# Kernel optimization log

Measured on AMD Instinct MI355X. Metric: run time of the kernel, lower is better.

## Reference

```python
import jax, jax.numpy as jnp
import numpy as np
from jax import lax


def quick_gelu(x):
    return x * jax.nn.sigmoid(1.702 * x)


def setup_inputs() -> dict:
    key = jax.random.key(0)
    ks = jax.random.split(key, 12)
    B, H, W, C, D, M = 32, 56, 56, 192, 64, 8
    g = lambda k, shape, s: (jax.random.normal(k, shape, jnp.float32) * s)
    return {
        "x": jax.random.normal(ks[0], (B, H, W, C), jnp.float32),
        "W1": g(ks[1], (64, C), 0.05),
        "b1": jnp.zeros((64,), jnp.float32),
        "W2": g(ks[2], (64, 64), 0.05),
        "b2": jnp.zeros((64,), jnp.float32),
        "mask_token": g(ks[3], (M, 64), 0.05),
        "Wh": g(ks[4], (D * D * 9, 64), 0.02),
        "bh": g(ks[5], (D * D * 9,), 0.02),
        "Wd": g(ks[6], (D, C), 0.05),
        "bd": jnp.zeros((D,), jnp.float32),
        "Wu": g(ks[7], (C, D), 0.02),
        "bu": jnp.zeros((C,), jnp.float32),
    }


def reference(x, W1, b1, W2, b2, mask_token, Wh, bh, Wd, bd, Wu, bu):
    B, H, W_, C = x.shape
    D = Wd.shape[0]
    M = mask_token.shape[0]
    # meta_net: Linear -> ReLU -> Linear, [B,H,W,64]
    pf = jax.nn.relu(jnp.einsum("bhwc,kc->bhwk", x, W1) + b1)
    pf = jnp.einsum("bhwk,jk->bhwj", pf, W2) + b2
    # mask routing: [M,B,H,W], softmax over spatial positions
    mask = jnp.einsum("bhwk,mk->mbhw", pf, mask_token)
    mask = jax.nn.softmax(mask.reshape(M, B, -1), axis=-1).reshape(M, B, H, W_)
    # sum_m mask[m][...,None]*pf, then sum over H,W -> [B,64]
    mwf = (mask.sum(0)[..., None] * pf).sum(axis=(1, 2))
    # hypernet: per-sample conv weights [B,D,D,3,3]
    conv_w = (jnp.einsum("bk,ok->bo", mwf, Wh) + bh).reshape(B, D, D, 3, 3)
    # adapter_down + QuickGELU, [B,D,H,W]
    xd = jnp.einsum("bhwc,dc->bhwd", x, Wd) + bd
    xp = quick_gelu(xd.transpose(0, 3, 1, 2))

    def conv1(xi, wi):  # xi [D,H,W], wi [D,D,3,3]
        return lax.conv_general_dilated(xi[None], wi, (1, 1), [(1, 1), (1, 1)])[0]

    xc = jax.vmap(conv1)(xp, conv_w)  # [B,D,H,W]
    xd2 = quick_gelu(xc.transpose(0, 2, 3, 1))  # [B,H,W,D]
    # dropout(p=0.1) is identity in eval mode
    xu = jnp.einsum("bhwd,cd->bhwc", xd2, Wu) + bu
    return xu + x
```

## Files before the change

kernel.cpp:

```cpp
#include <hip/hip_runtime.h>

typedef unsigned short ushort_t;
typedef short bf16x8 __attribute__((ext_vector_type(8)));
typedef float f32x4 __attribute__((ext_vector_type(4)));

#define MFMA(a, b, c) __builtin_amdgcn_mfma_f32_16x16x32_bf16(a, b, c, 0, 0, 0)

#define B_    32
#define HW_   3136
#define NPOS  100352

__device__ __forceinline__ float bf2f(unsigned short h) {
    return __uint_as_float(((unsigned int)h) << 16);
}
__device__ __forceinline__ unsigned short f2bf(float f) {
    unsigned int u = __float_as_uint(f);
    u += 0x7FFFu + ((u >> 16) & 1u);
    return (unsigned short)(u >> 16);
}
__device__ __forceinline__ float qgelu(float v) {
    return v / (1.0f + __expf(-1.702f * v));
}
__device__ __forceinline__ void unpack8(uint4 v, float* f) {
    f[0] = bf2f((unsigned short)(v.x & 0xffff)); f[1] = bf2f((unsigned short)(v.x >> 16));
    f[2] = bf2f((unsigned short)(v.y & 0xffff)); f[3] = bf2f((unsigned short)(v.y >> 16));
    f[4] = bf2f((unsigned short)(v.z & 0xffff)); f[5] = bf2f((unsigned short)(v.z >> 16));
    f[6] = bf2f((unsigned short)(v.w & 0xffff)); f[7] = bf2f((unsigned short)(v.w >> 16));
}

__global__ __launch_bounds__(256) void k0_prep(
    const float* __restrict__ W1, const float* __restrict__ W2,
    const float* __restrict__ mtok, const float* __restrict__ Wd,
    const float* __restrict__ Wu,
    ushort_t* __restrict__ w1f, ushort_t* __restrict__ wdf,
    ushort_t* __restrict__ w2f, ushort_t* __restrict__ mtf,
    ushort_t* __restrict__ wuf)
{
    const int gid = blockIdx.x * 256 + threadIdx.x;
    const int stride = gridDim.x * 256;
    for (int i = gid; i < 12288; i += stride) {
        int j = i & 7, lane = (i >> 3) & 63, nt = (i >> 9) & 3, kc = i >> 11;
        int n = nt * 16 + (lane & 15), k = kc * 32 + (lane >> 4) * 8 + j;
        w1f[i] = f2bf(W1[n * 192 + k]);
        wdf[i] = f2bf(Wd[n * 192 + k]);
    }
    for (int i = gid; i < 4096; i += stride) {
        int j = i & 7, lane = (i >> 3) & 63, nt = (i >> 9) & 3, kc = i >> 11;
        int n = nt * 16 + (lane & 15), k = kc * 32 + (lane >> 4) * 8 + j;
        w2f[i] = f2bf(W2[n * 64 + k]);
    }
    for (int i = gid; i < 1024; i += stride) {
        int j = i & 7, lane = (i >> 3) & 63, kc = i >> 9;
        int n = lane & 15, k = kc * 32 + (lane >> 4) * 8 + j;
        mtf[i] = (n < 8) ? f2bf(mtok[n * 64 + k]) : (ushort_t)0;
    }
    for (int i = gid; i < 12288; i += stride) {
        int j = i & 7, lane = (i >> 3) & 63, g = i >> 9;
        int nt = g % 12, kc = g / 12;
        int n = nt * 16 + (lane & 15), k = kc * 32 + (lane >> 4) * 8 + j;
        wuf[i] = f2bf(Wu[n * 64 + k]);
    }
}

__global__ __launch_bounds__(256) void k1_meta_adapter(
    const float* __restrict__ x, const float* __restrict__ b1,
    const float* __restrict__ b2, const float* __restrict__ bd,
    const ushort_t* __restrict__ w1f, const ushort_t* __restrict__ wdf,
    const ushort_t* __restrict__ w2f, const ushort_t* __restrict__ mtf,
    ushort_t* __restrict__ pf2g, ushort_t* __restrict__ xpg,
    float* __restrict__ Lg)
{
    __shared__ ushort_t xs[64 * 200];
    __shared__ ushort_t pf1s[4][16 * 72];

    const int tid = threadIdx.x;
    const int posBase = blockIdx.x * 64;

    #pragma unroll
    for (int t = 0; t < 6; t++) {
        int u = tid + t * 256;
        int pos = u / 24, c8 = u % 24;
        const float4* gp = (const float4*)(x + ((size_t)(posBase + pos)) * 192 + c8 * 8);
        float4 v0 = gp[0], v1 = gp[1];
        bf16x8 r;
        r[0] = (short)f2bf(v0.x); r[1] = (short)f2bf(v0.y);
        r[2] = (short)f2bf(v0.z); r[3] = (short)f2bf(v0.w);
        r[4] = (short)f2bf(v1.x); r[5] = (short)f2bf(v1.y);
        r[6] = (short)f2bf(v1.z); r[7] = (short)f2bf(v1.w);
        *(bf16x8*)&xs[pos * 200 + c8 * 8] = r;
    }
    __syncthreads();

    const int lane = tid & 63, wv = tid >> 6;
    const int col = lane & 15, q = lane >> 4;

    bf16x8 A[6];
    #pragma unroll
    for (int kc = 0; kc < 6; kc++)
        A[kc] = *(const bf16x8*)&xs[(wv * 16 + col) * 200 + kc * 32 + q * 8];

    f32x4 acc1[4], acc3[4];
    #pragma unroll
    for (int nt = 0; nt < 4; nt++) { acc1[nt] = (f32x4)0.0f; acc3[nt] = (f32x4)0.0f; }

    #pragma unroll
    for (int kc = 0; kc < 6; kc++) {
        #pragma unroll
        for (int nt = 0; nt < 4; nt++) {
            bf16x8 B1 = *(const bf16x8*)(w1f + ((kc * 4 + nt) * 64 + lane) * 8);
            acc1[nt] = MFMA(A[kc], B1, acc1[nt]);
            bf16x8 Bd = *(const bf16x8*)(wdf + ((kc * 4 + nt) * 64 + lane) * 8);
            acc3[nt] = MFMA(A[kc], Bd, acc3[nt]);
        }
    }
    __syncthreads();

    #pragma unroll
    for (int nt = 0; nt < 4; nt++) {
        float bias = b1[nt * 16 + col];
        #pragma unroll
        for (int r = 0; r < 4; r++) {
            float v = acc1[nt][r] + bias;
            v = v > 0.0f ? v : 0.0f;
            pf1s[wv][(q * 4 + r) * 72 + nt * 16 + col] = f2bf(v);
        }
    }

    f32x4 acc2[4];
    #pragma unroll
    for (int nt = 0; nt < 4; nt++) acc2[nt] = (f32x4)0.0f;
    #pragma unroll
    for (int kc = 0; kc < 2; kc++) {
        bf16x8 A2 = *(const bf16x8*)&pf1s[wv][col * 72 + kc * 32 + q * 8];
        #pragma unroll
        for (int nt = 0; nt < 4; nt++) {
            bf16x8 B2 = *(const bf16x8*)(w2f + ((kc * 4 + nt) * 64 + lane) * 8);
            acc2[nt] = MFMA(A2, B2, acc2[nt]);
        }
    }

    #pragma unroll
    for (int nt = 0; nt < 4; nt++) {
        float bias = bd[nt * 16 + col];
        #pragma unroll
        for (int r = 0; r < 4; r++) {
            float v = qgelu(acc3[nt][r] + bias);
            xs[(wv * 16 + q * 4 + r) * 72 + nt * 16 + col] = f2bf(v);
        }
    }

    #pragma unroll
    for (int nt = 0; nt < 4; nt++) {
        float bias = b2[nt * 16 + col];
        #pragma unroll
        for (int r = 0; r < 4; r++)
            pf1s[wv][(q * 4 + r) * 72 + nt * 16 + col] = f2bf(acc2[nt][r] + bias);
    }

    f32x4 Lacc = (f32x4)0.0f;
    #pragma unroll
    for (int kc = 0; kc < 2; kc++) {
        bf16x8 A3 = *(const bf16x8*)&pf1s[wv][col * 72 + kc * 32 + q * 8];
        bf16x8 Bm = *(const bf16x8*)(mtf + (kc * 64 + lane) * 8);
        Lacc = MFMA(A3, Bm, Lacc);
    }
    if (col < 8) {
        #pragma unroll
        for (int r = 0; r < 4; r++)
            Lg[((size_t)(posBase + wv * 16 + q * 4 + r)) * 8 + col] = Lacc[r];
    }
    __syncthreads();

    #pragma unroll
    for (int t = 0; t < 2; t++) {
        int u = tid + t * 256;
        int pos = u >> 3, c8 = u & 7;
        uint4 vx = *(const uint4*)&xs[pos * 72 + c8 * 8];
        *(uint4*)(xpg + ((size_t)(posBase + pos)) * 64 + c8 * 8) = vx;
        uint4 vp = *(const uint4*)&pf1s[pos >> 4][(pos & 15) * 72 + c8 * 8];
        *(uint4*)(pf2g + ((size_t)(posBase + pos)) * 64 + c8 * 8) = vp;
    }
}

__global__ __launch_bounds__(256) void k2_mask_mwf(
    const float* __restrict__ Lg, const ushort_t* __restrict__ pf2g,
    float* __restrict__ mwfg)
{
    __shared__ float masksum[HW_];
    __shared__ float wred[4][8];
    __shared__ float smx[8];
    __shared__ float sinv[8];
    __shared__ float sred[32 * 64];

    const int tid = threadIdx.x;
    const int b = blockIdx.x;
    const int lane = tid & 63, wv = tid >> 6;
    const float* Lb = Lg + (size_t)b * HW_ * 8;

    float lmax[8];
    #pragma unroll
    for (int m = 0; m < 8; m++) lmax[m] = -1e30f;
    for (int p = tid; p < HW_; p += 256) {
        const float4* lp = (const float4*)(Lb + (size_t)p * 8);
        float4 a = lp[0], c = lp[1];
        lmax[0] = fmaxf(lmax[0], a.x); lmax[1] = fmaxf(lmax[1], a.y);
        lmax[2] = fmaxf(lmax[2], a.z); lmax[3] = fmaxf(lmax[3], a.w);
        lmax[4] = fmaxf(lmax[4], c.x); lmax[5] = fmaxf(lmax[5], c.y);
        lmax[6] = fmaxf(lmax[6], c.z); lmax[7] = fmaxf(lmax[7], c.w);
    }
    #pragma unroll
    for (int m = 0; m < 8; m++) {
        float v = lmax[m];
        for (int off = 32; off > 0; off >>= 1) v = fmaxf(v, __shfl_down(v, off));
        lmax[m] = v;
    }
    if (lane == 0) {
        #pragma unroll
        for (int m = 0; m < 8; m++) wred[wv][m] = lmax[m];
    }
    __syncthreads();
    if (tid < 8)
        smx[tid] = fmaxf(fmaxf(wred[0][tid], wred[1][tid]), fmaxf(wred[2][tid], wred[3][tid]));
    __syncthreads();

    float lsum[8];
    #pragma unroll
    for (int m = 0; m < 8; m++) lsum[m] = 0.0f;
    for (int p = tid; p < HW_; p += 256) {
        const float4* lp = (const float4*)(Lb + (size_t)p * 8);
        float4 a = lp[0], c = lp[1];
        lsum[0] += __expf(a.x - smx[0]); lsum[1] += __expf(a.y - smx[1]);
        lsum[2] += __expf(a.z - smx[2]); lsum[3] += __expf(a.w - smx[3]);
        lsum[4] += __expf(c.x - smx[4]); lsum[5] += __expf(c.y - smx[5]);
        lsum[6] += __expf(c.z - smx[6]); lsum[7] += __expf(c.w - smx[7]);
    }
    #pragma unroll
    for (int m = 0; m < 8; m++) {
        float v = lsum[m];
        for (int off = 32; off > 0; off >>= 1) v += __shfl_down(v, off);
        lsum[m] = v;
    }
    __syncthreads();
    if (lane == 0) {
        #pragma unroll
        for (int m = 0; m < 8; m++) wred[wv][m] = lsum[m];
    }
    __syncthreads();
    if (tid < 8)
        sinv[tid] = 1.0f / (wred[0][tid] + wred[1][tid] + wred[2][tid] + wred[3][tid]);
    __syncthreads();

    for (int p = tid; p < HW_; p += 256) {
        const float4* lp = (const float4*)(Lb + (size_t)p * 8);
        float4 a = lp[0], c = lp[1];
        float ms = __expf(a.x - smx[0]) * sinv[0] + __expf(a.y - smx[1]) * sinv[1]
                 + __expf(a.z - smx[2]) * sinv[2] + __expf(a.w - smx[3]) * sinv[3]
                 + __expf(c.x - smx[4]) * sinv[4] + __expf(c.y - smx[5]) * sinv[5]
                 + __expf(c.z - smx[6]) * sinv[6] + __expf(c.w - smx[7]) * sinv[7];
        masksum[p] = ms;
    }
    __syncthreads();

    const int part = tid >> 3, kg = tid & 7;
    float a8[8];
    #pragma unroll
    for (int j = 0; j < 8; j++) a8[j] = 0.0f;
    for (int p = part; p < HW_; p += 32) {
        float ms = masksum[p];
        uint4 v = *(const uint4*)(pf2g + ((size_t)b * HW_ + p) * 64 + kg * 8);
        float f[8]; unpack8(v, f);
        #pragma unroll
        for (int j = 0; j < 8; j++) a8[j] += ms * f[j];
    }
    #pragma unroll
    for (int j = 0; j < 8; j++) sred[part * 64 + kg * 8 + j] = a8[j];
    __syncthreads();
    if (tid < 64) {
        float s = 0.0f;
        #pragma unroll
        for (int pt = 0; pt < 32; pt++) s += sred[pt * 64 + tid];
        mwfg[b * 64 + tid] = s;
    }
}

__global__ __launch_bounds__(256) void k3_hypernet(
    const float* __restrict__ mwfg, const float* __restrict__ Whg,
    const float* __restrict__ bhg, ushort_t* __restrict__ cwb)
{
    __shared__ float mwfs[32 * 64];
    const int tid = threadIdx.x;
    for (int i = tid; i < 2048; i += 256) mwfs[i] = mwfg[i];
    __syncthreads();

    const int op = blockIdx.x * 256 + tid;
    const int j = op & 7, lane = (op >> 3) & 63, nt = (op >> 9) & 3;
    const int kc = (op >> 11) & 1, tap = op >> 12;
    const int oc = nt * 16 + (lane & 15);
    const int ic = kc * 32 + (lane >> 4) * 8 + j;
    const int o = oc * 576 + ic * 9 + tap;

    float wreg[64];
    const float4* src = (const float4*)(Whg + (size_t)o * 64);
    #pragma unroll
    for (int t = 0; t < 16; t++) {
        float4 v = src[t];
        wreg[t * 4 + 0] = v.x; wreg[t * 4 + 1] = v.y;
        wreg[t * 4 + 2] = v.z; wreg[t * 4 + 3] = v.w;
    }
    const float bias = bhg[o];
    for (int b = 0; b < 32; b++) {
        float a = bias;
        #pragma unroll
        for (int k = 0; k < 64; k++) a += mwfs[b * 64 + k] * wreg[k];
        cwb[(size_t)b * 36864 + op] = f2bf(a);
    }
}

__global__ __launch_bounds__(256, 4) void k4_conv(
    const ushort_t* __restrict__ xpg, const ushort_t* __restrict__ cwb,
    ushort_t* __restrict__ xd2g)
{
    __shared__ ushort_t xs[2 * 232 * 40];

    const int tid = threadIdx.x;
    const int bid = blockIdx.x;
    const int swz = (bid & 7) * 112 + (bid >> 3);
    const int b = swz / 28, yt = swz % 28, y0 = yt * 2;

    for (int u = tid; u < 1856; u += 256) {
        int r = u / 464, rem = u % 464, c = rem >> 3, c8 = rem & 7;
        int gy = y0 - 1 + r, gx = c - 1;
        uint4 v = make_uint4(0, 0, 0, 0);
        if (gy >= 0 && gy < 56 && gx >= 0 && gx < 56)
            v = *(const uint4*)(xpg + ((size_t)b * HW_ + gy * 56 + gx) * 64 + c8 * 8);
        int kc = c8 >> 2, q = c8 & 3;
        *(uint4*)&xs[kc * 9280 + (r * 58 + c) * 40 + q * 8] = v;
    }
    __syncthreads();

    const int lane = tid & 63, wv = tid >> 6;
    const int col = lane & 15, q = lane >> 4;

    int abase[7];
    #pragma unroll
    for (int t = 0; t < 7; t++) {
        int p = t * 16 + col;
        int row = p / 56, cc = p - row * 56;
        abase[t] = ((row * 58 + cc) * 40 + q * 8) * 2;
    }

    f32x4 acc[7];
    #pragma unroll
    for (int t = 0; t < 7; t++) acc[t] = (f32x4)0.0f;

    const ushort_t* wbase = cwb + (size_t)b * 36864;
    #pragma unroll
    for (int tap = 0; tap < 9; tap++) {
        const int dy = tap / 3, dx = tap % 3;
        const int toff = (dy * 58 + dx) * 80;
        bf16x8 Bf0 = *(const bf16x8*)(wbase + tap * 4096 + ((0 * 4 + wv) * 64 + lane) * 8);
        bf16x8 Bf1 = *(const bf16x8*)(wbase + tap * 4096 + ((1 * 4 + wv) * 64 + lane) * 8);
        #pragma unroll
        for (int t = 0; t < 7; t++) {
            bf16x8 A0 = *(const bf16x8*)((const char*)xs + abase[t] + toff);
            bf16x8 A1 = *(const bf16x8*)((const char*)xs + 18560 + abase[t] + toff);
            acc[t] = MFMA(A0, Bf0, acc[t]);
            acc[t] = MFMA(A1, Bf1, acc[t]);
        }
    }
    __syncthreads();

    #pragma unroll
    for (int t = 0; t < 7; t++)
        #pragma unroll
        for (int r = 0; r < 4; r++)
            xs[(t * 16 + q * 4 + r) * 72 + wv * 16 + col] = f2bf(qgelu(acc[t][r]));
    __syncthreads();

    for (int u = tid; u < 896; u += 256) {
        int pos = u >> 3, c8 = u & 7;
        uint4 v = *(const uint4*)&xs[pos * 72 + c8 * 8];
        size_t gpos = (size_t)b * HW_ + (size_t)y0 * 56 + pos;
        *(uint4*)(xd2g + gpos * 64 + c8 * 8) = v;
    }
}

__global__ __launch_bounds__(256) void k5_up_res(
    const ushort_t* __restrict__ xd2g, const ushort_t* __restrict__ wuf,
    const float* __restrict__ bu, const float* __restrict__ xg,
    float* __restrict__ outg)
{
    __shared__ ushort_t xds[64 * 72];

    const int tid = threadIdx.x;
    const size_t posBase = (size_t)blockIdx.x * 64;

    #pragma unroll
    for (int t = 0; t < 2; t++) {
        int u = tid + t * 256;
        int pos = u >> 3, c8 = u & 7;
        uint4 v = *(const uint4*)(xd2g + (posBase + pos) * 64 + c8 * 8);
        *(uint4*)&xds[pos * 72 + c8 * 8] = v;
    }
    __syncthreads();

    const int lane = tid & 63, wv = tid >> 6;
    const int col = lane & 15, q = lane >> 4;

    bf16x8 A[2];
    #pragma unroll
    for (int kc = 0; kc < 2; kc++)
        A[kc] = *(const bf16x8*)&xds[(wv * 16 + col) * 72 + kc * 32 + q * 8];

    f32x4 acc[12];
    #pragma unroll
    for (int nt = 0; nt < 12; nt++) acc[nt] = (f32x4)0.0f;
    #pragma unroll
    for (int kc = 0; kc < 2; kc++)
        #pragma unroll
        for (int nt = 0; nt < 12; nt++) {
            bf16x8 B = *(const bf16x8*)(wuf + ((kc * 12 + nt) * 64 + lane) * 8);
            acc[nt] = MFMA(A[kc], B, acc[nt]);
        }

    #pragma unroll
    for (int nt = 0; nt < 12; nt++) {
        float bias = bu[nt * 16 + col];
        #pragma unroll
        for (int r = 0; r < 4; r++) {
            size_t off = (posBase + wv * 16 + q * 4 + r) * 192 + nt * 16 + col;
            outg[off] = acc[nt][r] + bias + xg[off];
        }
    }
}

extern "C" void kernel_launch(void* const* d_in, const int* in_sizes, int n_in,
                              void* d_out, int out_size, void* d_ws, size_t ws_size,
                              hipStream_t stream) {
    const float* x    = (const float*)d_in[0];
    const float* W1   = (const float*)d_in[1];
    const float* b1   = (const float*)d_in[2];
    const float* W2   = (const float*)d_in[3];
    const float* b2   = (const float*)d_in[4];
    const float* mtok = (const float*)d_in[5];
    const float* Wh   = (const float*)d_in[6];
    const float* bh   = (const float*)d_in[7];
    const float* Wd   = (const float*)d_in[8];
    const float* bd   = (const float*)d_in[9];
    const float* Wu   = (const float*)d_in[10];
    const float* bu   = (const float*)d_in[11];
    float* out = (float*)d_out;

    char* ws = (char*)d_ws;
    ushort_t* pf2 = (ushort_t*)ws;
    ushort_t* xp  = (ushort_t*)(ws + 12845056);
    ushort_t* xd2 = pf2;
    ushort_t* cwb = (ushort_t*)(ws + 25690112);
    float*    mwf = (float*)(ws + 28049408);
    float*    Lg  = (float*)(ws + 28057600);
    ushort_t* w1f = (ushort_t*)(ws + 31268864);
    ushort_t* wdf = (ushort_t*)(ws + 31293440);
    ushort_t* w2f = (ushort_t*)(ws + 31318016);
    ushort_t* mtf = (ushort_t*)(ws + 31326208);
    ushort_t* wuf = (ushort_t*)(ws + 31328256);

    k0_prep<<<48, 256, 0, stream>>>(W1, W2, mtok, Wd, Wu, w1f, wdf, w2f, mtf, wuf);
    k1_meta_adapter<<<1568, 256, 0, stream>>>(x, b1, b2, bd, w1f, wdf, w2f, mtf,
                                              pf2, xp, Lg);
    k2_mask_mwf<<<32, 256, 0, stream>>>(Lg, pf2, mwf);
    k3_hypernet<<<144, 256, 0, stream>>>(mwf, Wh, bh, cwb);
    k4_conv<<<896, 256, 0, stream>>>(xp, cwb, xd2);
    k5_up_res<<<1568, 256, 0, stream>>>(xd2, wuf, bu, x, out);
}
```

Measured before the change: 269.4 us.

## Split softmax-mask reduction across 256 blocks and load x directly into registers

The per-batch mask softmax and weighted feature reduction, previously run by only 32 blocks, is split into three kernels: partial max/sum per 392-position slice, a combine step, and a sliced weighted sum accumulated with atomics. This spreads a serial, low-occupancy reduction over many more blocks. Separately, k1 now loads x rows straight from global into MFMA A registers with bf16 conversion, dropping the large shared staging tile and its block-wide barriers, and uses per-wave LDS buffers. The costs are two extra launches, float atomics that make the summation order nondeterministic, and less coalesced global reads of x.

```diff
diff --git a/kernel.cpp b/kernel.cpp
--- a/kernel.cpp
+++ b/kernel.cpp
@@ -70,34 +70,14 @@
     ushort_t* __restrict__ pf2g, ushort_t* __restrict__ xpg,
     float* __restrict__ Lg)
 {
-    __shared__ ushort_t xs[64 * 200];
-    __shared__ ushort_t pf1s[4][16 * 72];
-
-    const int tid = threadIdx.x;
-    const int posBase = blockIdx.x * 64;
-
-    #pragma unroll
-    for (int t = 0; t < 6; t++) {
-        int u = tid + t * 256;
-        int pos = u / 24, c8 = u % 24;
-        const float4* gp = (const float4*)(x + ((size_t)(posBase + pos)) * 192 + c8 * 8);
-        float4 v0 = gp[0], v1 = gp[1];
-        bf16x8 r;
-        r[0] = (short)f2bf(v0.x); r[1] = (short)f2bf(v0.y);
-        r[2] = (short)f2bf(v0.z); r[3] = (short)f2bf(v0.w);
-        r[4] = (short)f2bf(v1.x); r[5] = (short)f2bf(v1.y);
-        r[6] = (short)f2bf(v1.z); r[7] = (short)f2bf(v1.w);
-        *(bf16x8*)&xs[pos * 200 + c8 * 8] = r;
-    }
-    __syncthreads();
-
+    __shared__ ushort_t buf[4][2][16 * 72];
+
+    const int tid = threadIdx.x;
     const int lane = tid & 63, wv = tid >> 6;
     const int col = lane & 15, q = lane >> 4;
-
-    bf16x8 A[6];
-    #pragma unroll
-    for (int kc = 0; kc < 6; kc++)
-        A[kc] = *(const bf16x8*)&xs[(wv * 16 + col) * 200 + kc * 32 + q * 8];
+    const int posBase = blockIdx.x * 64;
+    const int myrow = posBase + wv * 16 + col;
+    const float* xrow = x + (size_t)myrow * 192;
 
     f32x4 acc1[4], acc3[4];
     #pragma unroll
@@ -105,15 +85,24 @@
 
     #pragma unroll
     for (int kc = 0; kc < 6; kc++) {
+        const float4* gp = (const float4*)(xrow + kc * 32 + q * 8);
+        float4 v0 = gp[0], v1 = gp[1];
+        bf16x8 A;
+        A[0] = (short)f2bf(v0.x); A[1] = (short)f2bf(v0.y);
+        A[2] = (short)f2bf(v0.z); A[3] = (short)f2bf(v0.w);
+        A[4] = (short)f2bf(v1.x); A[5] = (short)f2bf(v1.y);
+        A[6] = (short)f2bf(v1.z); A[7] = (short)f2bf(v1.w);
         #pragma unroll
         for (int nt = 0; nt < 4; nt++) {
             bf16x8 B1 = *(const bf16x8*)(w1f + ((kc * 4 + nt) * 64 + lane) * 8);
-            acc1[nt] = MFMA(A[kc], B1, acc1[nt]);
+            acc1[nt] = MFMA(A, B1, acc1[nt]);
             bf16x8 Bd = *(const bf16x8*)(wdf + ((kc * 4 + nt) * 64 + lane) * 8);
-            acc3[nt] = MFMA(A[kc], Bd, acc3[nt]);
-        }
-    }
-    __syncthreads();
+            acc3[nt] = MFMA(A, Bd, acc3[nt]);
+        }
+    }
+
+    ushort_t* bA = &buf[wv][0][0];
+    ushort_t* bB = &buf[wv][1][0];
 
     #pragma unroll
     for (int nt = 0; nt < 4; nt++) {
@@ -122,7 +111,7 @@
         for (int r = 0; r < 4; r++) {
             float v = acc1[nt][r] + bias;
             v = v > 0.0f ? v : 0.0f;
-            pf1s[wv][(q * 4 + r) * 72 + nt * 16 + col] = f2bf(v);
+            bA[(q * 4 + r) * 72 + nt * 16 + col] = f2bf(v);
         }
     }
 
@@ -131,7 +120,7 @@
     for (int nt = 0; nt < 4; nt++) acc2[nt] = (f32x4)0.0f;
     #pragma unroll
     for (int kc = 0; kc < 2; kc++) {
-        bf16x8 A2 = *(const bf16x8*)&pf1s[wv][col * 72 + kc * 32 + q * 8];
+        bf16x8 A2 = *(const bf16x8*)&bA[col * 72 + kc * 32 + q * 8];
         #pragma unroll
         for (int nt = 0; nt < 4; nt++) {
             bf16x8 B2 = *(const bf16x8*)(w2f + ((kc * 4 + nt) * 64 + lane) * 8);
@@ -145,7 +134,7 @@
         #pragma unroll
         for (int r = 0; r < 4; r++) {
             float v = qgelu(acc3[nt][r] + bias);
-            xs[(wv * 16 + q * 4 + r) * 72 + nt * 16 + col] = f2bf(v);
+            bA[(q * 4 + r) * 72 + nt * 16 + col] = f2bf(v);
         }
     }
 
@@ -154,13 +143,13 @@
         float bias = b2[nt * 16 + col];
         #pragma unroll
         for (int r = 0; r < 4; r++)
-            pf1s[wv][(q * 4 + r) * 72 + nt * 16 + col] = f2bf(acc2[nt][r] + bias);
+            bB[(q * 4 + r) * 72 + nt * 16 + col] = f2bf(acc2[nt][r] + bias);
     }
 
     f32x4 Lacc = (f32x4)0.0f;
     #pragma unroll
     for (int kc = 0; kc < 2; kc++) {
-        bf16x8 A3 = *(const bf16x8*)&pf1s[wv][col * 72 + kc * 32 + q * 8];
+        bf16x8 A3 = *(const bf16x8*)&bB[col * 72 + kc * 32 + q * 8];
         bf16x8 Bm = *(const bf16x8*)(mtf + (kc * 64 + lane) * 8);
         Lacc = MFMA(A3, Bm, Lacc);
     }
@@ -169,95 +158,131 @@
         for (int r = 0; r < 4; r++)
             Lg[((size_t)(posBase + wv * 16 + q * 4 + r)) * 8 + col] = Lacc[r];
     }
-    __syncthreads();
 
     #pragma unroll
     for (int t = 0; t < 2; t++) {
-        int u = tid + t * 256;
-        int pos = u >> 3, c8 = u & 7;
-        uint4 vx = *(const uint4*)&xs[pos * 72 + c8 * 8];
-        *(uint4*)(xpg + ((size_t)(posBase + pos)) * 64 + c8 * 8) = vx;
-        uint4 vp = *(const uint4*)&pf1s[pos >> 4][(pos & 15) * 72 + c8 * 8];
-        *(uint4*)(pf2g + ((size_t)(posBase + pos)) * 64 + c8 * 8) = vp;
-    }
-}
-
-__global__ __launch_bounds__(256) void k2_mask_mwf(
+        int idx = lane + t * 64;
+        int pos = idx >> 3, c8 = idx & 7;
+        size_t gp = (size_t)(posBase + wv * 16 + pos);
+        uint4 vx = *(const uint4*)&bA[pos * 72 + c8 * 8];
+        *(uint4*)(xpg + gp * 64 + c8 * 8) = vx;
+        uint4 vp = *(const uint4*)&bB[pos * 72 + c8 * 8];
+        *(uint4*)(pf2g + gp * 64 + c8 * 8) = vp;
+    }
+}
+
+__global__ __launch_bounds__(256) void k2a_partial(
+    const float* __restrict__ Lg, float* __restrict__ Pmax, float* __restrict__ Psum)
+{
+    __shared__ float wred[4][8];
+    __shared__ float Msh[8];
+
+    const int tid = threadIdx.x;
+    const int b = blockIdx.x >> 3, sl = blockIdx.x & 7;
+    const int lane = tid & 63, wv = tid >> 6;
+    const float* Lb = Lg + ((size_t)b * HW_ + (size_t)sl * 392) * 8;
+
+    float l0[8], l1[8];
+    {
+        const float4* p = (const float4*)(Lb + (size_t)tid * 8);
+        float4 a = p[0], c = p[1];
+        l0[0] = a.x; l0[1] = a.y; l0[2] = a.z; l0[3] = a.w;
+        l0[4] = c.x; l0[5] = c.y; l0[6] = c.z; l0[7] = c.w;
+    }
+    if (tid < 136) {
+        const float4* p = (const float4*)(Lb + (size_t)(tid + 256) * 8);
+        float4 a = p[0], c = p[1];
+        l1[0] = a.x; l1[1] = a.y; l1[2] = a.z; l1[3] = a.w;
+        l1[4] = c.x; l1[5] = c.y; l1[6] = c.z; l1[7] = c.w;
+    } else {
+        #pragma unroll
+        for (int m = 0; m < 8; m++) l1[m] = -1e30f;
+    }
+
+    float lm[8];
+    #pragma unroll
+    for (int m = 0; m < 8; m++) {
+        float v = fmaxf(l0[m], l1[m]);
+        for (int off = 32; off > 0; off >>= 1) v = fmaxf(v, __shfl_down(v, off));
+        lm[m] = v;
+    }
+    if (lane == 0) {
+        #pragma unroll
+        for (int m = 0; m < 8; m++) wred[wv][m] = lm[m];
+    }
+    __syncthreads();
+    if (tid < 8)
+        Msh[tid] = fmaxf(fmaxf(wred[0][tid], wred[1][tid]), fmaxf(wred[2][tid], wred[3][tid]));
+    __syncthreads();
+
+    float s[8];
+    #pragma unroll
+    for (int m = 0; m < 8; m++)
+        s[m] = __expf(l0[m] - Msh[m]) + __expf(l1[m] - Msh[m]);
+    #pragma unroll
+    for (int m = 0; m < 8; m++) {
+        float v = s[m];
+        for (int off = 32; off > 0; off >>= 1) v += __shfl_down(v, off);
+        s[m] = v;
+    }
+    __syncthreads();
+    if (lane == 0) {
+        #pragma unroll
+        for (int m = 0; m < 8; m++) wred[wv][m] = s[m];
+    }
+    __syncthreads();
+    if (tid < 8) {
+        Psum[((size_t)b * 8 + sl) * 8 + tid] =
+            wred[0][tid] + wred[1][tid] + wred[2][tid] + wred[3][tid];
+        Pmax[((size_t)b * 8 + sl) * 8 + tid] = Msh[tid];
+    }
+}
+
+__global__ __launch_bounds__(256) void k2b_combine(
+    const float* __restrict__ Pmax, const float* __restrict__ Psum,
+    float* __restrict__ smxg, float* __restrict__ sinvg, float* __restrict__ mwfg)
+{
+    const int tid = threadIdx.x;
+    const int b = tid >> 3, m = tid & 7;
+    float M = -1e30f;
+    #pragma unroll
+    for (int sl = 0; sl < 8; sl++)
+        M = fmaxf(M, Pmax[((size_t)b * 8 + sl) * 8 + m]);
+    float S = 0.0f;
+    #pragma unroll
+    for (int sl = 0; sl < 8; sl++)
+        S += Psum[((size_t)b * 8 + sl) * 8 + m] * __expf(Pmax[((size_t)b * 8 + sl) * 8 + m] - M);
+    smxg[tid] = M;
+    sinvg[tid] = 1.0f / S;
+    for (int i = tid; i < 2048; i += 256) mwfg[i] = 0.0f;
+}
+
+__global__ __launch_bounds__(256) void k2c_mwf(
     const float* __restrict__ Lg, const ushort_t* __restrict__ pf2g,
+    const float* __restrict__ smxg, const float* __restrict__ sinvg,
     float* __restrict__ mwfg)
 {
-    __shared__ float masksum[HW_];
-    __shared__ float wred[4][8];
-    __shared__ float smx[8];
-    __shared__ float sinv[8];
+    __shared__ float ms[392];
     __shared__ float sred[32 * 64];
 
     const int tid = threadIdx.x;
-    const int b = blockIdx.x;
-    const int lane = tid & 63, wv = tid >> 6;
-    const float* Lb = Lg + (size_t)b * HW_ * 8;
-
-    float lmax[8];
-    #pragma unroll
-    for (int m = 0; m < 8; m++) lmax[m] = -1e30f;
-    for (int p = tid; p < HW_; p += 256) {
-        const float4* lp = (const float4*)(Lb + (size_t)p * 8);
-        float4 a = lp[0], c = lp[1];
-        lmax[0] = fmaxf(lmax[0], a.x); lmax[1] = fmaxf(lmax[1], a.y);
-        lmax[2] = fmaxf(lmax[2], a.z); lmax[3] = fmaxf(lmax[3], a.w);
-        lmax[4] = fmaxf(lmax[4], c.x); lmax[5] = fmaxf(lmax[5], c.y);
-        lmax[6] = fmaxf(lmax[6], c.z); lmax[7] = fmaxf(lmax[7], c.w);
-    }
+    const int b = blockIdx.x >> 3, sl = blockIdx.x & 7;
+    const size_t base = (size_t)b * HW_ + (size_t)sl * 392;
+
+    float smx[8], sinv[8];
     #pragma unroll
     for (int m = 0; m < 8; m++) {
-        float v = lmax[m];
-        for (int off = 32; off > 0; off >>= 1) v = fmaxf(v, __shfl_down(v, off));
-        lmax[m] = v;
-    }
-    if (lane == 0) {
-        #pragma unroll
-        for (int m = 0; m < 8; m++) wred[wv][m] = lmax[m];
-    }
-    __syncthreads();
-    if (tid < 8)
-        smx[tid] = fmaxf(fmaxf(wred[0][tid], wred[1][tid]), fmaxf(wred[2][tid], wred[3][tid]));
-    __syncthreads();
-
-    float lsum[8];
-    #pragma unroll
-    for (int m = 0; m < 8; m++) lsum[m] = 0.0f;
-    for (int p = tid; p < HW_; p += 256) {
-        const float4* lp = (const float4*)(Lb + (size_t)p * 8);
-        float4 a = lp[0], c = lp[1];
-        lsum[0] += __expf(a.x - smx[0]); lsum[1] += __expf(a.y - smx[1]);
-        lsum[2] += __expf(a.z - smx[2]); lsum[3] += __expf(a.w - smx[3]);
-        lsum[4] += __expf(c.x - smx[4]); lsum[5] += __expf(c.y - smx[5]);
-        lsum[6] += __expf(c.z - smx[6]); lsum[7] += __expf(c.w - smx[7]);
-    }
-    #pragma unroll
-    for (int m = 0; m < 8; m++) {
-        float v = lsum[m];
-        for (int off = 32; off > 0; off >>= 1) v += __shfl_down(v, off);
-        lsum[m] = v;
-    }
-    __syncthreads();
-    if (lane == 0) {
-        #pragma unroll
-        for (int m = 0; m < 8; m++) wred[wv][m] = lsum[m];
-    }
-    __syncthreads();
-    if (tid < 8)
-        sinv[tid] = 1.0f / (wred[0][tid] + wred[1][tid] + wred[2][tid] + wred[3][tid]);
-    __syncthreads();
-
-    for (int p = tid; p < HW_; p += 256) {
-        const float4* lp = (const float4*)(Lb + (size_t)p * 8);
-        float4 a = lp[0], c = lp[1];
-        float ms = __expf(a.x - smx[0]) * sinv[0] + __expf(a.y - smx[1]) * sinv[1]
-                 + __expf(a.z - smx[2]) * sinv[2] + __expf(a.w - smx[3]) * sinv[3]
-                 + __expf(c.x - smx[4]) * sinv[4] + __expf(c.y - smx[5]) * sinv[5]
-                 + __expf(c.z - smx[6]) * sinv[6] + __expf(c.w - smx[7]) * sinv[7];
-        masksum[p] = ms;
+        smx[m] = smxg[b * 8 + m];
+        sinv[m] = sinvg[b * 8 + m];
+    }
+
+    for (int lp = tid; lp < 392; lp += 256) {
+        const float4* p = (const float4*)(Lg + (base + lp) * 8);
+        float4 a = p[0], c = p[1];
+        ms[lp] = __expf(a.x - smx[0]) * sinv[0] + __expf(a.y - smx[1]) * sinv[1]
+               + __expf(a.z - smx[2]) * sinv[2] + __expf(a.w - smx[3]) * sinv[3]
+               + __expf(c.x - smx[4]) * sinv[4] + __expf(c.y - smx[5]) * sinv[5]
+               + __expf(c.z - smx[6]) * sinv[6] + __expf(c.w - smx[7]) * sinv[7];
     }
     __syncthreads();
 
@@ -265,12 +290,12 @@
     float a8[8];
     #pragma unroll
     for (int j = 0; j < 8; j++) a8[j] = 0.0f;
-    for (int p = part; p < HW_; p += 32) {
-        float ms = masksum[p];
-        uint4 v = *(const uint4*)(pf2g + ((size_t)b * HW_ + p) * 64 + kg * 8);
+    for (int lp = part; lp < 392; lp += 32) {
+        float w = ms[lp];
+        uint4 v = *(const uint4*)(pf2g + (base + lp) * 64 + kg * 8);
         float f[8]; unpack8(v, f);
         #pragma unroll
-        for (int j = 0; j < 8; j++) a8[j] += ms * f[j];
+        for (int j = 0; j < 8; j++) a8[j] += w * f[j];
     }
     #pragma unroll
     for (int j = 0; j < 8; j++) sred[part * 64 + kg * 8 + j] = a8[j];
@@ -279,7 +304,7 @@
         float s = 0.0f;
         #pragma unroll
         for (int pt = 0; pt < 32; pt++) s += sred[pt * 64 + tid];
-        mwfg[b * 64 + tid] = s;
+        atomicAdd(&mwfg[b * 64 + tid], s);
     }
 }
 
@@ -463,11 +488,17 @@
     ushort_t* w2f = (ushort_t*)(ws + 31318016);
     ushort_t* mtf = (ushort_t*)(ws + 31326208);
     ushort_t* wuf = (ushort_t*)(ws + 31328256);
+    float*    Pmax= (float*)(ws + 31352832);
+    float*    Psum= (float*)(ws + 31361024);
+    float*    smxg= (float*)(ws + 31369216);
+    float*    sinvg=(float*)(ws + 31370240);
 
     k0_prep<<<48, 256, 0, stream>>>(W1, W2, mtok, Wd, Wu, w1f, wdf, w2f, mtf, wuf);
     k1_meta_adapter<<<1568, 256, 0, stream>>>(x, b1, b2, bd, w1f, wdf, w2f, mtf,
                                               pf2, xp, Lg);
-    k2_mask_mwf<<<32, 256, 0, stream>>>(Lg, pf2, mwf);
+    k2a_partial<<<256, 256, 0, stream>>>(Lg, Pmax, Psum);
+    k2b_combine<<<1, 256, 0, stream>>>(Pmax, Psum, smxg, sinvg, mwf);
+    k2c_mwf<<<256, 256, 0, stream>>>(Lg, pf2, smxg, sinvg, mwf);
     k3_hypernet<<<144, 256, 0, stream>>>(mwf, Wh, bh, cwb);
     k4_conv<<<896, 256, 0, stream>>>(xp, cwb, xd2);
     k5_up_res<<<1568, 256, 0, stream>>>(xd2, wuf, bu, x, out);
```

Measured after the change: 243.3 us. -9.7%, faster.
